# Optimization experiments

Measured on AMD Instinct MI355X. Metric: run time of the kernel, lower is better.

Reference implementation:

```python
import jax, jax.numpy as jnp
import numpy as np
import math

B, L, HID, H = 4, 1024, 1024, 16
DH = HID // H              # 64
MAX_SEQ = 1024             # hard-coded in module


def setup_inputs() -> dict:
    key = jax.random.key(0)
    ks = jax.random.split(key, 6)
    s = 0.02  # small init scale (stands in for xavier)
    return {
        "x": jax.random.normal(ks[0], (B, L, HID), jnp.float32),
        "Wq": jax.random.normal(ks[1], (HID, HID), jnp.float32) * s,
        "bq": jnp.zeros((HID,), jnp.float32),
        "Wk": jax.random.normal(ks[2], (HID, HID), jnp.float32) * s,
        "bk": jnp.zeros((HID,), jnp.float32),
        "Wv": jax.random.normal(ks[3], (HID, HID), jnp.float32) * s,
        "bv": jnp.zeros((HID,), jnp.float32),
        "Wo": jax.random.normal(ks[4], (HID, HID), jnp.float32) * s,
        "bo": jnp.zeros((HID,), jnp.float32),
        "rel_emb": jax.random.normal(ks[5], (2 * MAX_SEQ - 1, DH), jnp.float32) * s,
    }


def reference(x, Wq, bq, Wk, bk, Wv, bv, Wo, bo, rel_emb):
    b, l, hid = x.shape
    dh = rel_emb.shape[1]
    h = hid // dh
    max_seq = (rel_emb.shape[0] + 1) // 2

    def heads(y):
        return y.reshape(b, l, h, dh).transpose(0, 2, 1, 3)  # [B,H,L,dh]

    q = heads(x @ Wq + bq)
    k = heads(x @ Wk + bk)
    v = heads(x @ Wv + bv)

    scores = jnp.einsum("bhid,bhjd->bhij", q, k) / math.sqrt(dh)
    scores = jnp.clip(scores, -100000.0, 100000.0)

    # relative position bias: rel_pos[i,j] = rel_emb[i - j + max_seq - 1]
    pos_idx = jnp.arange(l)[:, None] - jnp.arange(l)[None, :] + max_seq - 1
    rel_pos = rel_emb[pos_idx]                          # [L,L,dh]
    scores = scores + jnp.einsum("bhid,ijd->bhij", q, rel_pos)

    attn = jax.nn.softmax(scores, axis=-1)
    attn = attn / (attn.sum(axis=-1, keepdims=True) + 1e-8)  # faithful renorm
    # dropout is identity in eval mode

    ctx = jnp.einsum("bhij,bhjd->bhid", attn, v)
    ctx = ctx.transpose(0, 2, 1, 3).reshape(b, l, hid)
    return ctx @ Wo + bo
```

## Files before the change

### kernel.cpp

```cpp
#include <hip/hip_runtime.h>
#include <cstddef>

#define B_ 4
#define L_ 1024
#define H_ 16
#define DH_ 64
#define HID_ 1024
#define HEADSZ_ 4194304

typedef short bf16x8 __attribute__((ext_vector_type(8)));
typedef short bf16x4 __attribute__((ext_vector_type(4)));
typedef float f32x4  __attribute__((ext_vector_type(4)));

__device__ __forceinline__ short f2bf(float f) {
    unsigned u = __float_as_uint(f);
    u = (u + 0x7fffu + ((u >> 16) & 1u)) >> 16;
    return (short)u;
}
__device__ __forceinline__ float bf2f(short s) {
    return __uint_as_float(((unsigned)(unsigned short)s) << 16);
}
__device__ __forceinline__ void glds16(const short* g, short* l) {
    __builtin_amdgcn_global_load_lds(
        (const __attribute__((address_space(1))) unsigned int*)g,
        (__attribute__((address_space(3))) unsigned int*)l, 16, 0, 0);
}

__global__ __launch_bounds__(256) void xcast_k(
    const float* __restrict__ x, short* __restrict__ xb)
{
    const int base = (blockIdx.x * 256 + threadIdx.x) << 3;
    float4 f0 = *(const float4*)&x[base];
    float4 f1 = *(const float4*)&x[base + 4];
    bf16x8 p;
    p[0] = f2bf(f0.x); p[1] = f2bf(f0.y); p[2] = f2bf(f0.z); p[3] = f2bf(f0.w);
    p[4] = f2bf(f1.x); p[5] = f2bf(f1.y); p[6] = f2bf(f1.z); p[7] = f2bf(f1.w);
    *(bf16x8*)&xb[base] = p;
}

__global__ __launch_bounds__(256) void wcast4_k(
    const float* __restrict__ Wq, const float* __restrict__ Wk,
    const float* __restrict__ Wv, const float* __restrict__ Wo,
    short* __restrict__ Wt)
{
    const float* W = (blockIdx.z == 0) ? Wq : (blockIdx.z == 1) ? Wk
                   : (blockIdx.z == 2) ? Wv : Wo;
    short* dstb = Wt + (size_t)blockIdx.z * HID_ * HID_;
    __shared__ float T[64][65];
    const int t  = threadIdx.x;
    const int k0 = blockIdx.x << 6, n0 = blockIdx.y << 6;
    const int r  = t & 63;
    const int cg = t >> 6;
#pragma unroll
    for (int u = 0; u < 4; ++u) {
        float4 f = *(const float4*)&W[(size_t)(k0 + r) * HID_ + n0 + (cg << 4) + (u << 2)];
        T[r][(cg << 4) + (u << 2) + 0] = f.x;
        T[r][(cg << 4) + (u << 2) + 1] = f.y;
        T[r][(cg << 4) + (u << 2) + 2] = f.z;
        T[r][(cg << 4) + (u << 2) + 3] = f.w;
    }
    __syncthreads();
    bf16x8 p0, p1;
#pragma unroll
    for (int j = 0; j < 8; ++j) p0[j] = f2bf(T[(cg << 4) + j][r]);
#pragma unroll
    for (int j = 0; j < 8; ++j) p1[j] = f2bf(T[(cg << 4) + 8 + j][r]);
    short* dst = &dstb[(size_t)(n0 + r) * HID_ + k0 + (cg << 4)];
    *(bf16x8*)dst       = p0;
    *(bf16x8*)(dst + 8) = p1;
}

__global__ __launch_bounds__(256) void relcast_k(
    const float* __restrict__ rel, short* __restrict__ relimg)
{
    const int base = (blockIdx.x * 256 + threadIdx.x) << 3;
    if (base >= 2047 * 64) return;
    const int r = base >> 6, d0 = base & 63;
    float4 f0 = *(const float4*)&rel[base];
    float4 f1 = *(const float4*)&rel[base + 4];
    bf16x8 p;
    p[0] = f2bf(f0.x); p[1] = f2bf(f0.y); p[2] = f2bf(f0.z); p[3] = f2bf(f0.w);
    p[4] = f2bf(f1.x); p[5] = f2bf(f1.y); p[6] = f2bf(f1.z); p[7] = f2bf(f1.w);
    const size_t dst = ((size_t)(r >> 6) << 12) + ((r & 63) << 6)
                     + ((((d0 >> 3) ^ (r & 7))) << 3);
    *(bf16x8*)&relimg[dst] = p;
}

template <int NT>
__global__ __launch_bounds__(256, 2) void gemm_glds_k(
    const short* __restrict__ A, const short* __restrict__ Wt,
    const float* __restrict__ b0, const float* __restrict__ b1,
    const float* __restrict__ b2, void* __restrict__ outv,
    int K, int mode)
{
    constexpr int BN = NT * 32;
    __shared__ short As[128 * 32];
    __shared__ short Bs[BN * 32];

    const int t    = threadIdx.x;
    const int lane = t & 63, w = t >> 6;
    const int m0   = blockIdx.y << 7, n0 = blockIdx.x * BN;
    const int fr   = lane & 15, qd = lane >> 4;
    const int wm0  = (w & 1) << 6, wn0 = (w >> 1) * (NT << 4);

    f32x4 acc[4][NT];
#pragma unroll
    for (int i = 0; i < 4; ++i)
#pragma unroll
        for (int j = 0; j < NT; ++j) acc[i][j] = (f32x4){0.f, 0.f, 0.f, 0.f};

    const short* aSrc = A  + (size_t)(m0 + w * 32 + (lane >> 2)) * K + (lane & 3) * 8;
    const short* bSrc = Wt + (size_t)(n0 + w * (BN / 4) + (lane >> 2)) * K + (lane & 3) * 8;
    short* aDst0 = &As[(w * 32) * 32];
    short* aDst1 = &As[(w * 32 + 16) * 32];
    short* bDst0 = &Bs[(w * (BN / 4)) * 32];
    short* bDst1 = &Bs[(w * (BN / 4) + 16) * 32];

    for (int k0 = 0; k0 < K; k0 += 32) {
        __syncthreads();
        glds16(aSrc + k0, aDst0);
        glds16(aSrc + (size_t)16 * K + k0, aDst1);
        glds16(bSrc + k0, bDst0);
        if (NT == 4) glds16(bSrc + (size_t)16 * K + k0, bDst1);
        __syncthreads();

        bf16x8 af[4], bfv[NT];
#pragma unroll
        for (int mt = 0; mt < 4; ++mt)
            af[mt] = *(const bf16x8*)&As[(wm0 + (mt << 4) + fr) * 32 + (qd << 3)];
#pragma unroll
        for (int nt = 0; nt < NT; ++nt)
            bfv[nt] = *(const bf16x8*)&Bs[(wn0 + (nt << 4) + fr) * 32 + (qd << 3)];
#pragma unroll
        for (int mt = 0; mt < 4; ++mt)
#pragma unroll
            for (int nt = 0; nt < NT; ++nt)
                acc[mt][nt] = __builtin_amdgcn_mfma_f32_16x16x32_bf16(
                    af[mt], bfv[nt], acc[mt][nt], 0, 0, 0);
    }

#pragma unroll
    for (int nt = 0; nt < NT; ++nt) {
        const int coln = n0 + wn0 + (nt << 4) + fr;
        float bias;
        if (mode == 0) bias = b0[coln];
        else {
            const int t3 = coln >> 10;
            bias = (t3 == 0 ? b0 : t3 == 1 ? b1 : b2)[coln & 1023];
        }
#pragma unroll
        for (int mt = 0; mt < 4; ++mt)
#pragma unroll
            for (int rg = 0; rg < 4; ++rg) {
                const int row = m0 + wm0 + (mt << 4) + (qd << 2) + rg;
                const float val = acc[mt][nt][rg] + bias;
                if (mode == 0) {
                    ((float*)outv)[(size_t)row * HID_ + coln] = val;
                } else {
                    const int t3 = coln >> 10;
                    const int h  = (coln >> 6) & 15;
                    const int d  = coln & 63;
                    const int bb = row >> 10, l = row & 1023;
                    const size_t bhoff = ((size_t)(bb * H_ + h)) << 16;
                    size_t dst;
                    if (t3 == 0)
                        dst = bhoff + ((size_t)l << 6) + d;
                    else if (t3 == 1)
                        dst = (size_t)HEADSZ_ + bhoff + ((size_t)(l >> 6) << 12)
                            + ((l & 63) << 6) + ((((d >> 3) ^ (l & 7))) << 3) + (d & 7);
                    else
                        dst = 2 * (size_t)HEADSZ_ + bhoff + ((size_t)(l >> 6) << 12)
                            + ((size_t)d << 6) + (((((l >> 3) & 7) ^ (d & 7))) << 3) + (l & 7);
                    ((short*)outv)[dst] = f2bf(val);
                }
            }
    }
}

__global__ __launch_bounds__(256, 3) void attn_mfma_k(
    const short* __restrict__ q, const short* __restrict__ kimg,
    const short* __restrict__ vimg, const short* __restrict__ relimg,
    short* __restrict__ ctx)
{
    __shared__ __align__(16) short Ks[64 * 64];
    __shared__ __align__(16) short Vt[64 * 64];
    __shared__ __align__(16) short Rl[64 * 64];
    __shared__ __align__(16) short Ts[2 * 64 * 68];
    __shared__ __align__(16) short Ps[64 * 72];

    const int t    = threadIdx.x;
    const int i0   = blockIdx.x << 6;
    const int h    = blockIdx.y;
    const int b    = blockIdx.z;
    const size_t bh = (size_t)(b * H_ + h) << 16;
    const int lane = t & 63, w = t >> 6;
    const int fr   = lane & 15, qd = lane >> 4;
    const int m16  = i0 >> 6;
    const int iiB  = (w << 4) + (qd << 2);
    const int soff = w * 1024 + lane * 8;

    bf16x8 af[2];
#pragma unroll
    for (int hh = 0; hh < 2; ++hh)
        af[hh] = *(const bf16x8*)&q[bh + ((size_t)(i0 + (w << 4) + fr) << 6)
                                    + (((hh << 2) + qd) << 3)];

    glds16(relimg + ((size_t)(m16 + 16) << 12) + soff,       Rl + w * 1024);
    glds16(relimg + ((size_t)(m16 + 16) << 12) + soff + 512, Rl + w * 1024 + 512);
    __syncthreads();
    {
        f32x4 acc_t[4];
#pragma unroll
        for (int i = 0; i < 4; ++i) acc_t[i] = (f32x4){0.f, 0.f, 0.f, 0.f};
#pragma unroll
        for (int hh = 0; hh < 2; ++hh) {
            const int g = (hh << 2) + qd;
#pragma unroll
            for (int rt = 0; rt < 4; ++rt) {
                const int rr = (rt << 4) + fr;
                bf16x8 br = *(const bf16x8*)&Rl[(rr << 6) + ((g ^ (rr & 7)) << 3)];
                acc_t[rt] = __builtin_amdgcn_mfma_f32_16x16x32_bf16(af[hh], br, acc_t[rt], 0, 0, 0);
            }
        }
        const int pu = m16 & 1;
#pragma unroll
        for (int rt = 0; rt < 4; ++rt) {
            bf16x4 p;
            p[0] = f2bf(acc_t[rt][0]); p[1] = f2bf(acc_t[rt][1]);
            p[2] = f2bf(acc_t[rt][2]); p[3] = f2bf(acc_t[rt][3]);
            *(bf16x4*)&Ts[pu * 4352 + ((rt << 4) + fr) * 68 + iiB] = p;
        }
    }

    f32x4 acc_o[4];
#pragma unroll
    for (int i = 0; i < 4; ++i) acc_o[i] = (f32x4){0.f, 0.f, 0.f, 0.f};
    float den[4] = {0.f, 0.f, 0.f, 0.f};

    for (int jt = 0; jt < 16; ++jt) {
        const int mlow = m16 + 15 - jt;
        const int pl   = mlow & 1;

        __syncthreads();
        glds16(kimg + bh + ((size_t)jt << 12) + soff,       Ks + w * 1024);
        glds16(kimg + bh + ((size_t)jt << 12) + soff + 512, Ks + w * 1024 + 512);
        glds16(vimg + bh + ((size_t)jt << 12) + soff,       Vt + w * 1024);
        glds16(vimg + bh + ((size_t)jt << 12) + soff + 512, Vt + w * 1024 + 512);
        glds16(relimg + ((size_t)mlow << 12) + soff,        Rl + w * 1024);
        glds16(relimg + ((size_t)mlow << 12) + soff + 512,  Rl + w * 1024 + 512);
        __syncthreads();

        f32x4 acc_s[4];
#pragma unroll
        for (int i = 0; i < 4; ++i) acc_s[i] = (f32x4){0.f, 0.f, 0.f, 0.f};
#pragma unroll
        for (int hh = 0; hh < 2; ++hh) {
            const int g = (hh << 2) + qd;
#pragma unroll
            for (int nt = 0; nt < 4; ++nt) {
                const int rb = (nt << 4) + fr;
                bf16x8 bk = *(const bf16x8*)&Ks[(rb << 6) + ((g ^ (rb & 7)) << 3)];
                acc_s[nt] = __builtin_amdgcn_mfma_f32_16x16x32_bf16(af[hh], bk, acc_s[nt], 0, 0, 0);
            }
        }

        {
            f32x4 acc_t[4];
#pragma unroll
            for (int i = 0; i < 4; ++i) acc_t[i] = (f32x4){0.f, 0.f, 0.f, 0.f};
#pragma unroll
            for (int hh = 0; hh < 2; ++hh) {
                const int g = (hh << 2) + qd;
#pragma unroll
                for (int rt = 0; rt < 4; ++rt) {
                    const int rr = (rt << 4) + fr;
                    bf16x8 br = *(const bf16x8*)&Rl[(rr << 6) + ((g ^ (rr & 7)) << 3)];
                    acc_t[rt] = __builtin_amdgcn_mfma_f32_16x16x32_bf16(af[hh], br, acc_t[rt], 0, 0, 0);
                }
            }
#pragma unroll
            for (int rt = 0; rt < 4; ++rt) {
                bf16x4 p;
                p[0] = f2bf(acc_t[rt][0]); p[1] = f2bf(acc_t[rt][1]);
                p[2] = f2bf(acc_t[rt][2]); p[3] = f2bf(acc_t[rt][3]);
                *(bf16x4*)&Ts[pl * 4352 + ((rt << 4) + fr) * 68 + iiB] = p;
            }
        }

#pragma unroll
        for (int nt = 0; nt < 4; ++nt) {
            const int jj = (nt << 4) + fr;
#pragma unroll
            for (int rg = 0; rg < 4; ++rg) {
                const int ii = iiB + rg;
                const int r7 = ii - jj + 63;
                const int par = pl ^ (r7 >> 6);
                const float tv = bf2f(Ts[par * 4352 + (r7 & 63) * 68 + ii]);
                float s = acc_s[nt][rg] * 0.125f;
                s = fminf(fmaxf(s, -100000.f), 100000.f);
                const float e = __expf(s + tv);
                den[rg] += e;
                Ps[ii * 72 + jj] = f2bf(e);
            }
        }

#pragma unroll
        for (int hh = 0; hh < 2; ++hh) {
            const int g = (hh << 2) + qd;
            bf16x8 ap = *(const bf16x8*)&Ps[((w << 4) + fr) * 72 + (g << 3)];
#pragma unroll
            for (int nt = 0; nt < 4; ++nt) {
                const int rb = (nt << 4) + fr;
                bf16x8 bv = *(const bf16x8*)&Vt[(rb << 6) + ((g ^ (rb & 7)) << 3)];
                acc_o[nt] = __builtin_amdgcn_mfma_f32_16x16x32_bf16(ap, bv, acc_o[nt], 0, 0, 0);
            }
        }
    }

#pragma unroll
    for (int off = 1; off < 16; off <<= 1)
#pragma unroll
        for (int rg = 0; rg < 4; ++rg)
            den[rg] += __shfl_xor(den[rg], off);

#pragma unroll
    for (int rg = 0; rg < 4; ++rg) {
        const float inv = 1.0f / den[rg];
        const int l = i0 + iiB + rg;
#pragma unroll
        for (int nt = 0; nt < 4; ++nt)
            ctx[((size_t)(b * L_ + l) << 10) + (h << 6) + (nt << 4) + fr] =
                f2bf(acc_o[nt][rg] * inv);
    }
}

extern "C" void kernel_launch(void* const* d_in, const int* in_sizes, int n_in,
                              void* d_out, int out_size, void* d_ws, size_t ws_size,
                              hipStream_t stream)
{
    const float* x   = (const float*)d_in[0];
    const float* Wq  = (const float*)d_in[1];
    const float* bq  = (const float*)d_in[2];
    const float* Wk  = (const float*)d_in[3];
    const float* bk  = (const float*)d_in[4];
    const float* Wv  = (const float*)d_in[5];
    const float* bv  = (const float*)d_in[6];
    const float* Wo  = (const float*)d_in[7];
    const float* bo  = (const float*)d_in[8];
    const float* rel = (const float*)d_in[9];
    float* out = (float*)d_out;

    short* xb   = (short*)d_ws;
    short* qkv  = xb + (size_t)HEADSZ_;
    short* cw   = qkv + (size_t)3 * HEADSZ_;
    short* wt   = cw + (size_t)HEADSZ_;
    short* relimg = wt + (size_t)4 * HID_ * HID_;

    const dim3 tb(256);

    xcast_k<<<dim3(2048), tb, 0, stream>>>(x, xb);
    wcast4_k<<<dim3(16, 16, 4), tb, 0, stream>>>(Wq, Wk, Wv, Wo, wt);
    relcast_k<<<dim3(64), tb, 0, stream>>>(rel, relimg);

    gemm_glds_k<4><<<dim3(24, 32), tb, 0, stream>>>(
        xb, wt, bq, bk, bv, qkv, HID_, 1);

    attn_mfma_k<<<dim3(16, H_, B_), tb, 0, stream>>>(
        qkv, qkv + HEADSZ_, qkv + 2 * (size_t)HEADSZ_, relimg, cw);

    gemm_glds_k<2><<<dim3(16, 32), tb, 0, stream>>>(
        cw, wt + (size_t)3 * HID_ * HID_, bo, bo, bo, out, HID_, 0);
}
```

Measured before the change: 224.7 us.

## Merge cast kernels and deepen GEMM K-tile with XOR-swizzled LDS

The three prep cast kernels become one launch that picks its branch by block index. The GEMM now stages a 64-wide K slice per iteration with an XOR swizzle in LDS, which halves the barrier count and reduces bank conflicts. The output projection now uses 128x128 tiles instead of 128x64. That halves the grid for that GEMM to 256 blocks, which may underfill the CUs.

```diff
diff --git a/kernel.cpp b/kernel.cpp
--- a/kernel.cpp
+++ b/kernel.cpp
@@ -26,121 +26,127 @@
         (__attribute__((address_space(3))) unsigned int*)l, 16, 0, 0);
 }
 
-__global__ __launch_bounds__(256) void xcast_k(
-    const float* __restrict__ x, short* __restrict__ xb)
-{
-    const int base = (blockIdx.x * 256 + threadIdx.x) << 3;
-    float4 f0 = *(const float4*)&x[base];
-    float4 f1 = *(const float4*)&x[base + 4];
-    bf16x8 p;
-    p[0] = f2bf(f0.x); p[1] = f2bf(f0.y); p[2] = f2bf(f0.z); p[3] = f2bf(f0.w);
-    p[4] = f2bf(f1.x); p[5] = f2bf(f1.y); p[6] = f2bf(f1.z); p[7] = f2bf(f1.w);
-    *(bf16x8*)&xb[base] = p;
-}
-
-__global__ __launch_bounds__(256) void wcast4_k(
+__global__ __launch_bounds__(256) void prep_k(
+    const float* __restrict__ x,
     const float* __restrict__ Wq, const float* __restrict__ Wk,
     const float* __restrict__ Wv, const float* __restrict__ Wo,
-    short* __restrict__ Wt)
+    const float* __restrict__ rel,
+    short* __restrict__ xb, short* __restrict__ Wt, short* __restrict__ relimg)
 {
-    const float* W = (blockIdx.z == 0) ? Wq : (blockIdx.z == 1) ? Wk
-                   : (blockIdx.z == 2) ? Wv : Wo;
-    short* dstb = Wt + (size_t)blockIdx.z * HID_ * HID_;
-    __shared__ float T[64][65];
-    const int t  = threadIdx.x;
-    const int k0 = blockIdx.x << 6, n0 = blockIdx.y << 6;
-    const int r  = t & 63;
-    const int cg = t >> 6;
-#pragma unroll
-    for (int u = 0; u < 4; ++u) {
-        float4 f = *(const float4*)&W[(size_t)(k0 + r) * HID_ + n0 + (cg << 4) + (u << 2)];
-        T[r][(cg << 4) + (u << 2) + 0] = f.x;
-        T[r][(cg << 4) + (u << 2) + 1] = f.y;
-        T[r][(cg << 4) + (u << 2) + 2] = f.z;
-        T[r][(cg << 4) + (u << 2) + 3] = f.w;
-    }
-    __syncthreads();
-    bf16x8 p0, p1;
-#pragma unroll
-    for (int j = 0; j < 8; ++j) p0[j] = f2bf(T[(cg << 4) + j][r]);
-#pragma unroll
-    for (int j = 0; j < 8; ++j) p1[j] = f2bf(T[(cg << 4) + 8 + j][r]);
-    short* dst = &dstb[(size_t)(n0 + r) * HID_ + k0 + (cg << 4)];
-    *(bf16x8*)dst       = p0;
-    *(bf16x8*)(dst + 8) = p1;
-}
-
-__global__ __launch_bounds__(256) void relcast_k(
-    const float* __restrict__ rel, short* __restrict__ relimg)
-{
-    const int base = (blockIdx.x * 256 + threadIdx.x) << 3;
-    if (base >= 2047 * 64) return;
-    const int r = base >> 6, d0 = base & 63;
-    float4 f0 = *(const float4*)&rel[base];
-    float4 f1 = *(const float4*)&rel[base + 4];
-    bf16x8 p;
-    p[0] = f2bf(f0.x); p[1] = f2bf(f0.y); p[2] = f2bf(f0.z); p[3] = f2bf(f0.w);
-    p[4] = f2bf(f1.x); p[5] = f2bf(f1.y); p[6] = f2bf(f1.z); p[7] = f2bf(f1.w);
-    const size_t dst = ((size_t)(r >> 6) << 12) + ((r & 63) << 6)
-                     + ((((d0 >> 3) ^ (r & 7))) << 3);
-    *(bf16x8*)&relimg[dst] = p;
-}
-
-template <int NT>
+    const int bid = blockIdx.x;
+    const int t   = threadIdx.x;
+    if (bid < 2048) {
+        const int base = (bid * 256 + t) << 3;
+        float4 f0 = *(const float4*)&x[base];
+        float4 f1 = *(const float4*)&x[base + 4];
+        bf16x8 p;
+        p[0] = f2bf(f0.x); p[1] = f2bf(f0.y); p[2] = f2bf(f0.z); p[3] = f2bf(f0.w);
+        p[4] = f2bf(f1.x); p[5] = f2bf(f1.y); p[6] = f2bf(f1.z); p[7] = f2bf(f1.w);
+        *(bf16x8*)&xb[base] = p;
+    } else if (bid < 3072) {
+        const int idx = bid - 2048;
+        const int z = idx >> 8, tile = idx & 255;
+        const float* W = (z == 0) ? Wq : (z == 1) ? Wk : (z == 2) ? Wv : Wo;
+        short* dstb = Wt + (size_t)z * HID_ * HID_;
+        __shared__ float T[64][65];
+        const int k0 = (tile & 15) << 6, n0 = (tile >> 4) << 6;
+        const int r  = t & 63;
+        const int cg = t >> 6;
+#pragma unroll
+        for (int u = 0; u < 4; ++u) {
+            float4 f = *(const float4*)&W[(size_t)(k0 + r) * HID_ + n0 + (cg << 4) + (u << 2)];
+            T[r][(cg << 4) + (u << 2) + 0] = f.x;
+            T[r][(cg << 4) + (u << 2) + 1] = f.y;
+            T[r][(cg << 4) + (u << 2) + 2] = f.z;
+            T[r][(cg << 4) + (u << 2) + 3] = f.w;
+        }
+        __syncthreads();
+        bf16x8 p0, p1;
+#pragma unroll
+        for (int j = 0; j < 8; ++j) p0[j] = f2bf(T[(cg << 4) + j][r]);
+#pragma unroll
+        for (int j = 0; j < 8; ++j) p1[j] = f2bf(T[(cg << 4) + 8 + j][r]);
+        short* dst = &dstb[(size_t)(n0 + r) * HID_ + k0 + (cg << 4)];
+        *(bf16x8*)dst       = p0;
+        *(bf16x8*)(dst + 8) = p1;
+    } else {
+        const int base = ((bid - 3072) * 256 + t) << 3;
+        if (base >= 2047 * 64) return;
+        const int r = base >> 6, d0 = base & 63;
+        float4 f0 = *(const float4*)&rel[base];
+        float4 f1 = *(const float4*)&rel[base + 4];
+        bf16x8 p;
+        p[0] = f2bf(f0.x); p[1] = f2bf(f0.y); p[2] = f2bf(f0.z); p[3] = f2bf(f0.w);
+        p[4] = f2bf(f1.x); p[5] = f2bf(f1.y); p[6] = f2bf(f1.z); p[7] = f2bf(f1.w);
+        const size_t dst = ((size_t)(r >> 6) << 12) + ((r & 63) << 6)
+                         + ((((d0 >> 3) ^ (r & 7))) << 3);
+        *(bf16x8*)&relimg[dst] = p;
+    }
+}
+
 __global__ __launch_bounds__(256, 2) void gemm_glds_k(
     const short* __restrict__ A, const short* __restrict__ Wt,
     const float* __restrict__ b0, const float* __restrict__ b1,
     const float* __restrict__ b2, void* __restrict__ outv,
     int K, int mode)
 {
-    constexpr int BN = NT * 32;
-    __shared__ short As[128 * 32];
-    __shared__ short Bs[BN * 32];
+    __shared__ short As[128 * 64];
+    __shared__ short Bs[128 * 64];
 
     const int t    = threadIdx.x;
     const int lane = t & 63, w = t >> 6;
-    const int m0   = blockIdx.y << 7, n0 = blockIdx.x * BN;
+    const int m0   = blockIdx.y << 7, n0 = blockIdx.x << 7;
     const int fr   = lane & 15, qd = lane >> 4;
-    const int wm0  = (w & 1) << 6, wn0 = (w >> 1) * (NT << 4);
-
-    f32x4 acc[4][NT];
+    const int wm0  = (w & 1) << 6, wn0 = (w >> 1) << 6;
+
+    const int lr = lane >> 3;
+    const int sg = (lane & 7) ^ lr;
+
+    f32x4 acc[4][4];
 #pragma unroll
     for (int i = 0; i < 4; ++i)
 #pragma unroll
-        for (int j = 0; j < NT; ++j) acc[i][j] = (f32x4){0.f, 0.f, 0.f, 0.f};
-
-    const short* aSrc = A  + (size_t)(m0 + w * 32 + (lane >> 2)) * K + (lane & 3) * 8;
-    const short* bSrc = Wt + (size_t)(n0 + w * (BN / 4) + (lane >> 2)) * K + (lane & 3) * 8;
-    short* aDst0 = &As[(w * 32) * 32];
-    short* aDst1 = &As[(w * 32 + 16) * 32];
-    short* bDst0 = &Bs[(w * (BN / 4)) * 32];
-    short* bDst1 = &Bs[(w * (BN / 4) + 16) * 32];
-
-    for (int k0 = 0; k0 < K; k0 += 32) {
-        __syncthreads();
-        glds16(aSrc + k0, aDst0);
-        glds16(aSrc + (size_t)16 * K + k0, aDst1);
-        glds16(bSrc + k0, bDst0);
-        if (NT == 4) glds16(bSrc + (size_t)16 * K + k0, bDst1);
-        __syncthreads();
-
-        bf16x8 af[4], bfv[NT];
-#pragma unroll
-        for (int mt = 0; mt < 4; ++mt)
-            af[mt] = *(const bf16x8*)&As[(wm0 + (mt << 4) + fr) * 32 + (qd << 3)];
-#pragma unroll
-        for (int nt = 0; nt < NT; ++nt)
-            bfv[nt] = *(const bf16x8*)&Bs[(wn0 + (nt << 4) + fr) * 32 + (qd << 3)];
-#pragma unroll
-        for (int mt = 0; mt < 4; ++mt)
-#pragma unroll
-            for (int nt = 0; nt < NT; ++nt)
-                acc[mt][nt] = __builtin_amdgcn_mfma_f32_16x16x32_bf16(
-                    af[mt], bfv[nt], acc[mt][nt], 0, 0, 0);
-    }
-
-#pragma unroll
-    for (int nt = 0; nt < NT; ++nt) {
+        for (int j = 0; j < 4; ++j) acc[i][j] = (f32x4){0.f, 0.f, 0.f, 0.f};
+
+    const short* aBase = A  + (size_t)(m0 + w * 32 + lr) * K + sg * 8;
+    const short* bBase = Wt + (size_t)(n0 + w * 32 + lr) * K + sg * 8;
+    short* aDst = &As[(w * 32) * 64];
+    short* bDst = &Bs[(w * 32) * 64];
+
+    for (int k0 = 0; k0 < K; k0 += 64) {
+        __syncthreads();
+#pragma unroll
+        for (int g = 0; g < 4; ++g) {
+            glds16(aBase + (size_t)(g * 8) * K + k0, aDst + g * 8 * 64);
+            glds16(bBase + (size_t)(g * 8) * K + k0, bDst + g * 8 * 64);
+        }
+        __syncthreads();
+
+#pragma unroll
+        for (int hh2 = 0; hh2 < 2; ++hh2) {
+            const int kg = (hh2 << 2) + qd;
+            bf16x8 af[4], bfv[4];
+#pragma unroll
+            for (int mt = 0; mt < 4; ++mt) {
+                const int row = wm0 + (mt << 4) + fr;
+                af[mt] = *(const bf16x8*)&As[(row << 6) + ((kg ^ (row & 7)) << 3)];
+            }
+#pragma unroll
+            for (int nt = 0; nt < 4; ++nt) {
+                const int row = wn0 + (nt << 4) + fr;
+                bfv[nt] = *(const bf16x8*)&Bs[(row << 6) + ((kg ^ (row & 7)) << 3)];
+            }
+#pragma unroll
+            for (int mt = 0; mt < 4; ++mt)
+#pragma unroll
+                for (int nt = 0; nt < 4; ++nt)
+                    acc[mt][nt] = __builtin_amdgcn_mfma_f32_16x16x32_bf16(
+                        af[mt], bfv[nt], acc[mt][nt], 0, 0, 0);
+        }
+    }
+
+#pragma unroll
+    for (int nt = 0; nt < 4; ++nt) {
         const int coln = n0 + wn0 + (nt << 4) + fr;
         float bias;
         if (mode == 0) bias = b0[coln];
@@ -350,24 +356,22 @@
     const float* rel = (const float*)d_in[9];
     float* out = (float*)d_out;
 
-    short* xb   = (short*)d_ws;
-    short* qkv  = xb + (size_t)HEADSZ_;
-    short* cw   = qkv + (size_t)3 * HEADSZ_;
-    short* wt   = cw + (size_t)HEADSZ_;
+    short* xb     = (short*)d_ws;
+    short* qkv    = xb + (size_t)HEADSZ_;
+    short* cw     = qkv + (size_t)3 * HEADSZ_;
+    short* wt     = cw + (size_t)HEADSZ_;
     short* relimg = wt + (size_t)4 * HID_ * HID_;
 
     const dim3 tb(256);
 
-    xcast_k<<<dim3(2048), tb, 0, stream>>>(x, xb);
-    wcast4_k<<<dim3(16, 16, 4), tb, 0, stream>>>(Wq, Wk, Wv, Wo, wt);
-    relcast_k<<<dim3(64), tb, 0, stream>>>(rel, relimg);
-
-    gemm_glds_k<4><<<dim3(24, 32), tb, 0, stream>>>(
+    prep_k<<<dim3(3136), tb, 0, stream>>>(x, Wq, Wk, Wv, Wo, rel, xb, wt, relimg);
+
+    gemm_glds_k<<<dim3(24, 32), tb, 0, stream>>>(
         xb, wt, bq, bk, bv, qkv, HID_, 1);
 
     attn_mfma_k<<<dim3(16, H_, B_), tb, 0, stream>>>(
         qkv, qkv + HEADSZ_, qkv + 2 * (size_t)HEADSZ_, relimg, cw);
 
-    gemm_glds_k<2><<<dim3(16, 32), tb, 0, stream>>>(
+    gemm_glds_k<<<dim3(8, 32), tb, 0, stream>>>(
         cw, wt + (size_t)3 * HID_ * HID_, bo, bo, bo, out, HID_, 0);
 }
```

Result: no change. 225.4 us (+0.3%).
